# Performance work log

Measured on AMD Instinct MI355X. Metric: run time of the kernel, lower is better.

## Reference

```python
import jax, jax.numpy as jnp
import numpy as np

H = 512      # hidden_size
F = 1024     # expert_hidden_size
E = 16       # expert_count
EPS = 1e-5   # torch LayerNorm default eps


def setup_inputs() -> dict:
    key = jax.random.key(0)
    ks = jax.random.split(key, 7)
    tokens = jax.random.normal(ks[0], (4, 2048, H), dtype=jnp.float32)
    # Stacked per-expert parameters (one 3D tensor per parameter kind)
    ln_g = jnp.ones((E, H), dtype=jnp.float32)
    ln_b = jnp.zeros((E, H), dtype=jnp.float32)
    W1 = jax.random.normal(ks[1], (E, H, F), dtype=jnp.float32) * (1.0 / np.sqrt(H))
    b1 = jax.random.normal(ks[2], (E, F), dtype=jnp.float32) * 0.01
    W2 = jax.random.normal(ks[3], (E, F, H), dtype=jnp.float32) * (1.0 / np.sqrt(F))
    b2 = jax.random.normal(ks[4], (E, H), dtype=jnp.float32) * 0.01
    return {"tokens": tokens, "ln_g": ln_g, "ln_b": ln_b,
            "W1": W1, "b1": b1, "W2": W2, "b2": b2}


def reference(tokens, ln_g, ln_b, W1, b1, W2, b2):
    # LayerNorm statistics depend only on tokens, so compute x_hat once
    mu = jnp.mean(tokens, axis=-1, keepdims=True)
    var = jnp.mean(jnp.square(tokens - mu), axis=-1, keepdims=True)
    x_hat = (tokens - mu) * jax.lax.rsqrt(var + EPS)          # [B,S,H]
    # Per-expert affine: [B,S,E,H]
    xin = x_hat[:, :, None, :] * ln_g + ln_b
    h = jnp.einsum('bseh,ehf->bsef', xin, W1) + b1            # [B,S,E,F]
    h = jax.nn.gelu(h, approximate=False)                     # torch GELU default (erf)
    out = jnp.einsum('bsef,efh->bseh', h, W2) + b2            # [B,S,E,H] (stack dim=2)
    return out
```

## Files before the change

kernel.cpp:

```cpp
#include <hip/hip_runtime.h>
#include <stdint.h>

#define H 512
#define F 1024
#define E 16
#define TOK 8192
#define EPS 1e-5f

typedef short bf16x8 __attribute__((ext_vector_type(8)));
typedef float f32x4 __attribute__((ext_vector_type(4)));

__device__ __forceinline__ float bf2f(unsigned short u) {
    union { unsigned int i; float f; } v; v.i = ((unsigned int)u) << 16; return v.f;
}
__device__ __forceinline__ unsigned short f2bf(float f) {
    union { float f; unsigned int i; } v; v.f = f;
    unsigned int r = (v.i + 0x7FFFu + ((v.i >> 16) & 1u)) >> 16;
    return (unsigned short)r;
}
__device__ __forceinline__ void gload16(const void* g, void* l) {
    __builtin_amdgcn_global_load_lds(
        (const __attribute__((address_space(1))) unsigned int*)g,
        (__attribute__((address_space(3))) unsigned int*)l, 16, 0, 0);
}

__device__ __forceinline__ float gelu_erf(float v) {
    const float x  = v * 0.70710678118654752f;
    const float ax = fabsf(x);
    const float t  = __builtin_amdgcn_rcpf(fmaf(0.3275911f, ax, 1.0f));
    float p = fmaf(1.061405429f, t, -1.453152027f);
    p = fmaf(p, t, 1.421413741f);
    p = fmaf(p, t, -0.284496736f);
    p = fmaf(p, t, 0.254829592f);
    p = p * t;
    const float ex = __expf(-x * x);
    float er = fmaf(-p, ex, 1.0f);
    er = copysignf(er, x);
    return 0.5f * v * (1.0f + er);
}

__global__ void ln_kernel(const float* __restrict__ tokens,
                          unsigned short* __restrict__ xhat) {
    const int tid  = threadIdx.x;
    const int wid  = tid >> 6;
    const int lane = tid & 63;
    const int token = blockIdx.x * 4 + wid;

    const float* src = tokens + (size_t)token * H + lane * 8;
    float4 r0 = *reinterpret_cast<const float4*>(src);
    float4 r1 = *reinterpret_cast<const float4*>(src + 4);
    float x[8] = {r0.x, r0.y, r0.z, r0.w, r1.x, r1.y, r1.z, r1.w};

    float s = 0.f, s2 = 0.f;
#pragma unroll
    for (int j = 0; j < 8; ++j) { s += x[j]; s2 += x[j] * x[j]; }
#pragma unroll
    for (int m = 32; m >= 1; m >>= 1) {
        s  += __shfl_xor(s, m);
        s2 += __shfl_xor(s2, m);
    }
    const float mu  = s * (1.0f / H);
    float var = s2 * (1.0f / H) - mu * mu;
    var = fmaxf(var, 0.0f);
    const float rstd = rsqrtf(var + EPS);

    unsigned short o[8];
#pragma unroll
    for (int j = 0; j < 8; ++j) o[j] = f2bf((x[j] - mu) * rstd);
    uint4 w;
    w.x = o[0] | ((unsigned)o[1] << 16);
    w.y = o[2] | ((unsigned)o[3] << 16);
    w.z = o[4] | ((unsigned)o[5] << 16);
    w.w = o[6] | ((unsigned)o[7] << 16);
    *reinterpret_cast<uint4*>(xhat + (size_t)token * H + lane * 8) = w;
}

#define XPAD 72
__global__ void transpose_kernel(const float* __restrict__ src,
                                 unsigned short* __restrict__ dst,
                                 int rows, int cols,
                                 const float* __restrict__ scale) {
    __shared__ __align__(16) unsigned short tile[64 * XPAD];
    const int e  = blockIdx.z;
    const int r0 = blockIdx.y * 64;
    const int c0 = blockIdx.x * 64;
    const int tid = threadIdx.x;

    const float* sbase = src + (size_t)e * rows * cols;
    unsigned short* dbase = dst + (size_t)e * rows * cols;

    {
        const int r  = tid >> 2;
        const int cg = (tid & 3) * 16;
        const float* p = sbase + (size_t)(r0 + r) * cols + c0 + cg;
        const float sc = (scale != nullptr) ? scale[e * rows + r0 + r] : 1.0f;
        unsigned short u[16];
#pragma unroll
        for (int j = 0; j < 16; j += 4) {
            float4 v = *reinterpret_cast<const float4*>(p + j);
            u[j + 0] = f2bf(v.x * sc);
            u[j + 1] = f2bf(v.y * sc);
            u[j + 2] = f2bf(v.z * sc);
            u[j + 3] = f2bf(v.w * sc);
        }
#pragma unroll
        for (int j = 0; j < 16; j += 8) {
            uint4 w;
            w.x = u[j + 0] | ((unsigned)u[j + 1] << 16);
            w.y = u[j + 2] | ((unsigned)u[j + 3] << 16);
            w.z = u[j + 4] | ((unsigned)u[j + 5] << 16);
            w.w = u[j + 6] | ((unsigned)u[j + 7] << 16);
            *reinterpret_cast<uint4*>(&tile[r * XPAD + cg + j]) = w;
        }
    }
    __syncthreads();
#pragma unroll
    for (int i = 0; i < 2; ++i) {
        const int oc = (tid >> 3) + i * 32;
        const int og = (tid & 7) * 8;
        unsigned short u[8];
#pragma unroll
        for (int j = 0; j < 8; ++j) u[j] = tile[(og + j) * XPAD + oc];
        uint4 w;
        w.x = u[0] | ((unsigned)u[1] << 16);
        w.y = u[2] | ((unsigned)u[3] << 16);
        w.z = u[4] | ((unsigned)u[5] << 16);
        w.w = u[6] | ((unsigned)u[7] << 16);
        *reinterpret_cast<uint4*>(dbase + (size_t)(c0 + oc) * rows + r0 + og) = w;
    }
}

__global__ void b1fold_kernel(const float* __restrict__ b1,
                              const float* __restrict__ lnb,
                              const float* __restrict__ W1,
                              float* __restrict__ b1p) {
    __shared__ float slb[64];
    const int e = blockIdx.y;
    const int z = blockIdx.z;
    const int f = blockIdx.x * 256 + threadIdx.x;
    const int h0 = z * 64;
    if (threadIdx.x < 64) slb[threadIdx.x] = lnb[e * H + h0 + threadIdx.x];
    __syncthreads();
    float acc = (z == 0) ? b1[e * F + f] : 0.0f;
    const float* w = W1 + (size_t)e * H * F + (size_t)h0 * F + f;
#pragma unroll 8
    for (int h = 0; h < 64; ++h) acc += slb[h] * w[(size_t)h * F];
    atomicAdd(&b1p[e * F + f], acc);
}

__global__ __launch_bounds__(256, 3) void gemm1_kernel(
    const unsigned short* __restrict__ xhat,
    const unsigned short* __restrict__ w1gt,
    const float* __restrict__ b1p,
    unsigned short* __restrict__ hbuf)
{
    __shared__ __align__(16) unsigned short lds_x[128 * 64];
    __shared__ __align__(16) unsigned short lds_w[128 * 64];

    const int tid  = threadIdx.x;
    const int lane = tid & 63;
    const int wid  = tid >> 6;
    const int quad = lane >> 4;
    const int l16  = lane & 15;

    const unsigned bid = blockIdx.x;
    const int e  = bid & 15;
    const int t  = bid >> 4;
    const int ft = t & 7;
    const int mt = t >> 3;
    const int m0 = mt * 128, f0 = ft * 128;
    const int wm = wid & 1, wn = wid >> 1;

    f32x4 acc[4][4];
#pragma unroll
    for (int mi = 0; mi < 4; ++mi)
#pragma unroll
        for (int ni = 0; ni < 4; ++ni) acc[mi][ni] = (f32x4){0.f, 0.f, 0.f, 0.f};

    const unsigned short* xg = xhat + (size_t)m0 * H;
    const unsigned short* wg = w1gt + ((size_t)e * F + f0) * H;
    const int swzr = (l16 & 7) * 8;

    for (int kt = 0; kt < 8; ++kt) {
        const int k0 = kt * 64;
        __syncthreads();
#pragma unroll
        for (int i = 0; i < 4; ++i) {
            const int idx = tid + i * 256;
            const int row = idx >> 3;
            const int c   = ((idx & 7) * 8) ^ ((row & 7) * 8);
            gload16(xg + (size_t)row * H + k0 + c, (char*)lds_x + (size_t)idx * 16);
            gload16(wg + (size_t)row * H + k0 + c, (char*)lds_w + (size_t)idx * 16);
        }
        __syncthreads();
#pragma unroll
        for (int ks = 0; ks < 2; ++ks) {
            const int kc = (ks * 32 + quad * 8) ^ swzr;
            bf16x8 a[4], b[4];
#pragma unroll
            for (int i = 0; i < 4; ++i)
                a[i] = *reinterpret_cast<const bf16x8*>(&lds_x[(wm * 64 + i * 16 + l16) * 64 + kc]);
#pragma unroll
            for (int i = 0; i < 4; ++i)
                b[i] = *reinterpret_cast<const bf16x8*>(&lds_w[(wn * 64 + i * 16 + l16) * 64 + kc]);
#pragma unroll
            for (int mi = 0; mi < 4; ++mi)
#pragma unroll
                for (int ni = 0; ni < 4; ++ni)
                    acc[mi][ni] = __builtin_amdgcn_mfma_f32_16x16x32_bf16(a[mi], b[ni], acc[mi][ni], 0, 0, 0);
        }
    }

    float bv[4];
#pragma unroll
    for (int ni = 0; ni < 4; ++ni)
        bv[ni] = b1p[e * F + f0 + wn * 64 + ni * 16 + l16];
#pragma unroll
    for (int mi = 0; mi < 4; ++mi) {
#pragma unroll
        for (int r = 0; r < 4; ++r) {
            const int row = m0 + wm * 64 + mi * 16 + quad * 4 + r;
            unsigned short* dst = hbuf + ((size_t)row * E + e) * F + f0;
#pragma unroll
            for (int ni = 0; ni < 4; ++ni) {
                const float v = acc[mi][ni][r] + bv[ni];
                dst[wn * 64 + ni * 16 + l16] = f2bf(gelu_erf(v));
            }
        }
    }
}

__global__ __launch_bounds__(512, 4) void gemm2_kernel(
    const unsigned short* __restrict__ hbuf,
    const unsigned short* __restrict__ w2t,
    const float* __restrict__ b2,
    float* __restrict__ outp)
{
    __shared__ __align__(16) unsigned short lds_h[64 * 64];

    const int tid  = threadIdx.x;
    const int lane = tid & 63;
    const int wn   = tid >> 6;
    const int quad = lane >> 4;
    const int l16  = lane & 15;

    const int e  = blockIdx.x & 15;
    const int mt = blockIdx.x >> 4;
    const int m0 = mt * 64;

    f32x4 acc[4][4];
#pragma unroll
    for (int mi = 0; mi < 4; ++mi)
#pragma unroll
        for (int ni = 0; ni < 4; ++ni) acc[mi][ni] = (f32x4){0.f, 0.f, 0.f, 0.f};

    const unsigned short* hg = hbuf + ((size_t)m0 * E + e) * F;
    const unsigned short* wb = w2t + ((size_t)e * H + wn * 64 + l16) * F;
    const int swzr = (l16 & 7) * 8;

    for (int kt = 0; kt < 16; ++kt) {
        const int k0 = kt * 64;
        __syncthreads();
        {
            const int row = tid >> 3;
            const int c   = ((tid & 7) * 8) ^ ((row & 7) * 8);
            gload16(hg + (size_t)row * (E * F) + k0 + c, (char*)lds_h + (size_t)tid * 16);
        }
        __syncthreads();
#pragma unroll
        for (int ks = 0; ks < 2; ++ks) {
            const int kcb = ks * 32 + quad * 8;
            const int kc  = kcb ^ swzr;
            bf16x8 a[4];
#pragma unroll
            for (int i = 0; i < 4; ++i)
                a[i] = *reinterpret_cast<const bf16x8*>(&lds_h[(i * 16 + l16) * 64 + kc]);
#pragma unroll
            for (int ni = 0; ni < 4; ++ni) {
                const bf16x8 b = *reinterpret_cast<const bf16x8*>(
                    wb + (size_t)(ni * 16) * F + k0 + kcb);
#pragma unroll
                for (int mi = 0; mi < 4; ++mi)
                    acc[mi][ni] = __builtin_amdgcn_mfma_f32_16x16x32_bf16(a[mi], b, acc[mi][ni], 0, 0, 0);
            }
        }
    }

    float bv[4];
#pragma unroll
    for (int ni = 0; ni < 4; ++ni)
        bv[ni] = b2[e * H + wn * 64 + ni * 16 + l16];
#pragma unroll
    for (int mi = 0; mi < 4; ++mi) {
#pragma unroll
        for (int r = 0; r < 4; ++r) {
            const int row = m0 + mi * 16 + quad * 4 + r;
            float* dst = outp + ((size_t)row * E + e) * H;
#pragma unroll
            for (int ni = 0; ni < 4; ++ni)
                dst[wn * 64 + ni * 16 + l16] = acc[mi][ni][r] + bv[ni];
        }
    }
}

extern "C" void kernel_launch(void* const* d_in, const int* in_sizes, int n_in,
                              void* d_out, int out_size, void* d_ws, size_t ws_size,
                              hipStream_t stream) {
    const float* tokens = (const float*)d_in[0];
    const float* ln_g   = (const float*)d_in[1];
    const float* ln_b   = (const float*)d_in[2];
    const float* W1     = (const float*)d_in[3];
    const float* b1     = (const float*)d_in[4];
    const float* W2     = (const float*)d_in[5];
    const float* b2     = (const float*)d_in[6];

    char* ws = (char*)d_ws;
    unsigned short* xhat = (unsigned short*)(ws);
    unsigned short* w1gt = (unsigned short*)(ws + 8388608);
    unsigned short* w2t  = (unsigned short*)(ws + 25165824);
    float*          b1p  = (float*)(ws + 41943040);

    unsigned short* hbuf = (unsigned short*)d_out;
    float*          outp = (float*)d_out;

    hipMemsetAsync(b1p, 0, E * F * sizeof(float), stream);
    hipLaunchKernelGGL(ln_kernel, dim3(TOK / 4), dim3(256), 0, stream, tokens, xhat);
    hipLaunchKernelGGL(transpose_kernel, dim3(F / 64, H / 64, E), dim3(256), 0, stream,
                       W1, w1gt, H, F, ln_g);
    hipLaunchKernelGGL(transpose_kernel, dim3(H / 64, F / 64, E), dim3(256), 0, stream,
                       W2, w2t, F, H, (const float*)nullptr);
    hipLaunchKernelGGL(b1fold_kernel, dim3(F / 256, E, 8), dim3(256), 0, stream, b1, ln_b, W1, b1p);
    hipLaunchKernelGGL(gemm1_kernel, dim3(E * (TOK / 128) * (F / 128)), dim3(256), 0, stream,
                       xhat, w1gt, b1p, hbuf);
    hipLaunchKernelGGL(gemm2_kernel, dim3(E * (TOK / 64)), dim3(512), 0, stream,
                       hbuf, w2t, b2, outp);
}
```

Measured before the change: 796.0 us.

## Fuse both expert GEMMs into one kernel keeping GELU activations in LDS

Merges the two GEMM kernels into one 1024-thread block per (64-token tile, expert). The first GEMM's GELU output stays in a 128KB swizzled LDS buffer that the second GEMM reads directly, so the bf16 hidden tensor no longer goes through global memory. In exchange, W1 and W2 fragments are loaded straight from global without LDS staging, the large LDS footprint limits occupancy to one block per CU, and each block recomputes nothing but does no cross-block weight reuse.

Result: slower. 1.104 ms (+38.6%).

```diff
diff --git a/kernel.cpp b/kernel.cpp
--- a/kernel.cpp
+++ b/kernel.cpp
@@ -148,157 +148,137 @@
     atomicAdd(&b1p[e * F + f], acc);
 }
 
-__global__ __launch_bounds__(256, 3) void gemm1_kernel(
+__global__ __launch_bounds__(1024, 4) void fused_kernel(
     const unsigned short* __restrict__ xhat,
     const unsigned short* __restrict__ w1gt,
     const float* __restrict__ b1p,
-    unsigned short* __restrict__ hbuf)
-{
-    __shared__ __align__(16) unsigned short lds_x[128 * 64];
-    __shared__ __align__(16) unsigned short lds_w[128 * 64];
-
-    const int tid  = threadIdx.x;
-    const int lane = tid & 63;
-    const int wid  = tid >> 6;
-    const int quad = lane >> 4;
-    const int l16  = lane & 15;
-
-    const unsigned bid = blockIdx.x;
-    const int e  = bid & 15;
-    const int t  = bid >> 4;
-    const int ft = t & 7;
-    const int mt = t >> 3;
-    const int m0 = mt * 128, f0 = ft * 128;
-    const int wm = wid & 1, wn = wid >> 1;
-
-    f32x4 acc[4][4];
-#pragma unroll
-    for (int mi = 0; mi < 4; ++mi)
-#pragma unroll
-        for (int ni = 0; ni < 4; ++ni) acc[mi][ni] = (f32x4){0.f, 0.f, 0.f, 0.f};
-
-    const unsigned short* xg = xhat + (size_t)m0 * H;
-    const unsigned short* wg = w1gt + ((size_t)e * F + f0) * H;
-    const int swzr = (l16 & 7) * 8;
-
-    for (int kt = 0; kt < 8; ++kt) {
-        const int k0 = kt * 64;
-        __syncthreads();
-#pragma unroll
-        for (int i = 0; i < 4; ++i) {
-            const int idx = tid + i * 256;
-            const int row = idx >> 3;
-            const int c   = ((idx & 7) * 8) ^ ((row & 7) * 8);
-            gload16(xg + (size_t)row * H + k0 + c, (char*)lds_x + (size_t)idx * 16);
-            gload16(wg + (size_t)row * H + k0 + c, (char*)lds_w + (size_t)idx * 16);
-        }
-        __syncthreads();
-#pragma unroll
-        for (int ks = 0; ks < 2; ++ks) {
-            const int kc = (ks * 32 + quad * 8) ^ swzr;
-            bf16x8 a[4], b[4];
-#pragma unroll
-            for (int i = 0; i < 4; ++i)
-                a[i] = *reinterpret_cast<const bf16x8*>(&lds_x[(wm * 64 + i * 16 + l16) * 64 + kc]);
-#pragma unroll
-            for (int i = 0; i < 4; ++i)
-                b[i] = *reinterpret_cast<const bf16x8*>(&lds_w[(wn * 64 + i * 16 + l16) * 64 + kc]);
-#pragma unroll
-            for (int mi = 0; mi < 4; ++mi)
-#pragma unroll
-                for (int ni = 0; ni < 4; ++ni)
-                    acc[mi][ni] = __builtin_amdgcn_mfma_f32_16x16x32_bf16(a[mi], b[ni], acc[mi][ni], 0, 0, 0);
-        }
-    }
-
-    float bv[4];
-#pragma unroll
-    for (int ni = 0; ni < 4; ++ni)
-        bv[ni] = b1p[e * F + f0 + wn * 64 + ni * 16 + l16];
-#pragma unroll
-    for (int mi = 0; mi < 4; ++mi) {
-#pragma unroll
-        for (int r = 0; r < 4; ++r) {
-            const int row = m0 + wm * 64 + mi * 16 + quad * 4 + r;
-            unsigned short* dst = hbuf + ((size_t)row * E + e) * F + f0;
-#pragma unroll
-            for (int ni = 0; ni < 4; ++ni) {
-                const float v = acc[mi][ni][r] + bv[ni];
-                dst[wn * 64 + ni * 16 + l16] = f2bf(gelu_erf(v));
-            }
-        }
-    }
-}
-
-__global__ __launch_bounds__(512, 4) void gemm2_kernel(
-    const unsigned short* __restrict__ hbuf,
     const unsigned short* __restrict__ w2t,
     const float* __restrict__ b2,
     float* __restrict__ outp)
 {
-    __shared__ __align__(16) unsigned short lds_h[64 * 64];
+    __shared__ __align__(16) unsigned short lds_x[64 * 64];
+    __shared__ __align__(16) unsigned short lds_h[64 * 1024];
 
     const int tid  = threadIdx.x;
     const int lane = tid & 63;
-    const int wn   = tid >> 6;
+    const int w    = tid >> 6;
     const int quad = lane >> 4;
     const int l16  = lane & 15;
+    const int swzr = (l16 & 7) * 8;
 
     const int e  = blockIdx.x & 15;
     const int mt = blockIdx.x >> 4;
     const int m0 = mt * 64;
 
-    f32x4 acc[4][4];
-#pragma unroll
-    for (int mi = 0; mi < 4; ++mi)
-#pragma unroll
-        for (int ni = 0; ni < 4; ++ni) acc[mi][ni] = (f32x4){0.f, 0.f, 0.f, 0.f};
-
-    const unsigned short* hg = hbuf + ((size_t)m0 * E + e) * F;
-    const unsigned short* wb = w2t + ((size_t)e * H + wn * 64 + l16) * F;
-    const int swzr = (l16 & 7) * 8;
-
-    for (int kt = 0; kt < 16; ++kt) {
-        const int k0 = kt * 64;
-        __syncthreads();
-        {
-            const int row = tid >> 3;
-            const int c   = ((tid & 7) * 8) ^ ((row & 7) * 8);
-            gload16(hg + (size_t)row * (E * F) + k0 + c, (char*)lds_h + (size_t)tid * 16);
-        }
-        __syncthreads();
-#pragma unroll
-        for (int ks = 0; ks < 2; ++ks) {
-            const int kcb = ks * 32 + quad * 8;
-            const int kc  = kcb ^ swzr;
-            bf16x8 a[4];
-#pragma unroll
-            for (int i = 0; i < 4; ++i)
-                a[i] = *reinterpret_cast<const bf16x8*>(&lds_h[(i * 16 + l16) * 64 + kc]);
-#pragma unroll
-            for (int ni = 0; ni < 4; ++ni) {
-                const bf16x8 b = *reinterpret_cast<const bf16x8*>(
-                    wb + (size_t)(ni * 16) * F + k0 + kcb);
+    {
+        f32x4 acc[4][4];
+#pragma unroll
+        for (int mi = 0; mi < 4; ++mi)
+#pragma unroll
+            for (int ni = 0; ni < 4; ++ni) acc[mi][ni] = (f32x4){0.f, 0.f, 0.f, 0.f};
+
+        const int fw = w * 64;
+        const unsigned short* xg = xhat + (size_t)m0 * H;
+        const unsigned short* wg = w1gt + ((size_t)e * F + fw) * H;
+
+        for (int kt = 0; kt < 8; ++kt) {
+            const int k0 = kt * 64;
+            __syncthreads();
+            if (tid < 512) {
+                const int row = tid >> 3;
+                const int c   = ((tid & 7) * 8) ^ ((row & 7) * 8);
+                gload16(xg + (size_t)row * H + k0 + c, (char*)lds_x + (size_t)tid * 16);
+            }
+            __syncthreads();
+#pragma unroll
+            for (int ks = 0; ks < 2; ++ks) {
+                const int kcb = ks * 32 + quad * 8;
+                const int kc  = kcb ^ swzr;
+                bf16x8 a[4], b[4];
 #pragma unroll
                 for (int mi = 0; mi < 4; ++mi)
-                    acc[mi][ni] = __builtin_amdgcn_mfma_f32_16x16x32_bf16(a[mi], b, acc[mi][ni], 0, 0, 0);
-            }
-        }
-    }
-
-    float bv[4];
-#pragma unroll
-    for (int ni = 0; ni < 4; ++ni)
-        bv[ni] = b2[e * H + wn * 64 + ni * 16 + l16];
-#pragma unroll
-    for (int mi = 0; mi < 4; ++mi) {
-#pragma unroll
-        for (int r = 0; r < 4; ++r) {
-            const int row = m0 + mi * 16 + quad * 4 + r;
-            float* dst = outp + ((size_t)row * E + e) * H;
-#pragma unroll
-            for (int ni = 0; ni < 4; ++ni)
-                dst[wn * 64 + ni * 16 + l16] = acc[mi][ni][r] + bv[ni];
+                    a[mi] = *reinterpret_cast<const bf16x8*>(&lds_x[(mi * 16 + l16) * 64 + kc]);
+#pragma unroll
+                for (int ni = 0; ni < 4; ++ni)
+                    b[ni] = *reinterpret_cast<const bf16x8*>(
+                        wg + (size_t)(ni * 16 + l16) * H + k0 + kcb);
+#pragma unroll
+                for (int mi = 0; mi < 4; ++mi)
+#pragma unroll
+                    for (int ni = 0; ni < 4; ++ni)
+                        acc[mi][ni] = __builtin_amdgcn_mfma_f32_16x16x32_bf16(a[mi], b[ni], acc[mi][ni], 0, 0, 0);
+            }
+        }
+
+        float bv[4];
+#pragma unroll
+        for (int ni = 0; ni < 4; ++ni)
+            bv[ni] = b1p[e * F + fw + ni * 16 + l16];
+#pragma unroll
+        for (int mi = 0; mi < 4; ++mi) {
+#pragma unroll
+            for (int r = 0; r < 4; ++r) {
+                const int m = mi * 16 + quad * 4 + r;
+#pragma unroll
+                for (int ni = 0; ni < 4; ++ni) {
+                    const int f = fw + ni * 16 + l16;
+                    const float v = acc[mi][ni][r] + bv[ni];
+                    lds_h[m * 1024 + (f ^ ((m & 7) << 3))] = f2bf(gelu_erf(v));
+                }
+            }
+        }
+    }
+    __syncthreads();
+
+    {
+        const int mw = w & 1;
+        const int nw = w >> 1;
+
+        f32x4 acc[2][4];
+#pragma unroll
+        for (int mi = 0; mi < 2; ++mi)
+#pragma unroll
+            for (int ni = 0; ni < 4; ++ni) acc[mi][ni] = (f32x4){0.f, 0.f, 0.f, 0.f};
+
+        const unsigned short* wb = w2t + ((size_t)e * H + nw * 64 + l16) * F;
+        float bv[4];
+#pragma unroll
+        for (int ni = 0; ni < 4; ++ni)
+            bv[ni] = b2[e * H + nw * 64 + ni * 16 + l16];
+
+#pragma unroll 2
+        for (int kt = 0; kt < 16; ++kt) {
+            const int k0 = kt * 64;
+#pragma unroll
+            for (int ks = 0; ks < 2; ++ks) {
+                const int kcb = k0 + ks * 32 + quad * 8;
+                bf16x8 a[2], b[4];
+#pragma unroll
+                for (int mi = 0; mi < 2; ++mi) {
+                    const int m = mw * 32 + mi * 16 + l16;
+                    a[mi] = *reinterpret_cast<const bf16x8*>(&lds_h[m * 1024 + (kcb ^ swzr)]);
+                }
+#pragma unroll
+                for (int ni = 0; ni < 4; ++ni)
+                    b[ni] = *reinterpret_cast<const bf16x8*>(wb + (size_t)(ni * 16) * F + kcb);
+#pragma unroll
+                for (int mi = 0; mi < 2; ++mi)
+#pragma unroll
+                    for (int ni = 0; ni < 4; ++ni)
+                        acc[mi][ni] = __builtin_amdgcn_mfma_f32_16x16x32_bf16(a[mi], b[ni], acc[mi][ni], 0, 0, 0);
+            }
+        }
+
+#pragma unroll
+        for (int mi = 0; mi < 2; ++mi) {
+#pragma unroll
+            for (int r = 0; r < 4; ++r) {
+                const int row = m0 + mw * 32 + mi * 16 + quad * 4 + r;
+                float* dst = outp + ((size_t)row * E + e) * H + nw * 64;
+#pragma unroll
+                for (int ni = 0; ni < 4; ++ni)
+                    dst[ni * 16 + l16] = acc[mi][ni][r] + bv[ni];
+            }
         }
     }
 }
@@ -320,8 +300,7 @@
     unsigned short* w2t  = (unsigned short*)(ws + 25165824);
     float*          b1p  = (float*)(ws + 41943040);
 
-    unsigned short* hbuf = (unsigned short*)d_out;
-    float*          outp = (float*)d_out;
+    float* outp = (float*)d_out;
 
     hipMemsetAsync(b1p, 0, E * F * sizeof(float), stream);
     hipLaunchKernelGGL(ln_kernel, dim3(TOK / 4), dim3(256), 0, stream, tokens, xhat);
@@ -330,8 +309,6 @@
     hipLaunchKernelGGL(transpose_kernel, dim3(H / 64, F / 64, E), dim3(256), 0, stream,
                        W2, w2t, F, H, (const float*)nullptr);
     hipLaunchKernelGGL(b1fold_kernel, dim3(F / 256, E, 8), dim3(256), 0, stream, b1, ln_b, W1, b1p);
-    hipLaunchKernelGGL(gemm1_kernel, dim3(E * (TOK / 128) * (F / 128)), dim3(256), 0, stream,
-                       xhat, w1gt, b1p, hbuf);
-    hipLaunchKernelGGL(gemm2_kernel, dim3(E * (TOK / 64)), dim3(512), 0, stream,
-                       hbuf, w2t, b2, outp);
-}
+    hipLaunchKernelGGL(fused_kernel, dim3(E * (TOK / 64)), dim3(1024), 0, stream,
+                       xhat, w1gt, b1p, w2t, b2, outp);
+}
```
